# Kernel tuning notes

Measured on AMD Instinct MI355X. Metric: run time of the kernel, lower is better.

The kernel has to match this reference:

```python
import jax, jax.numpy as jnp
import numpy as np

B, X, Y, C, H = 16, 64, 64, 256, 8
N = X * Y
EPS_LN, EPS_BN = 1e-6, 1e-5

def _conv3x3(x, w):
    return jax.lax.conv_general_dilated(x, w, (1, 1), 'SAME', dimension_numbers=('NCHW', 'OIHW', 'NCHW'))

def _bn(x, g, b, m, v):
    # eval-mode BatchNorm2d with running stats
    s = g / jnp.sqrt(v + EPS_BN)
    return x * s[None, :, None, None] + (b - m * s)[None, :, None, None]

def _ln(x, g, b):
    mu = jnp.mean(x, -1, keepdims=True)
    var = jnp.mean((x - mu) ** 2, -1, keepdims=True)
    return (x - mu) * jax.lax.rsqrt(var + EPS_LN) * g + b

def _rotate_half(x):
    x1, x2 = jnp.split(x, 2, axis=-1)
    return jnp.concatenate([-x2, x1], axis=-1)

def _rope(t, f):
    return t * jnp.cos(f) + _rotate_half(t) * jnp.sin(f)

def setup_inputs() -> dict:
    key = jax.random.key(0)
    ks = jax.random.split(key, 9)
    p = {}
    p['input'] = jax.random.normal(ks[0], (B, X, Y), jnp.float32)
    p['freq_x'] = jax.random.normal(ks[1], (B, N, C // 2), jnp.float32)
    p['freq_y'] = jax.random.normal(ks[2], (B, N, C // 2), jnp.float32)
    p['conv1_w'] = jax.random.normal(ks[3], (C, 1, 3, 3), jnp.float32) * 0.1
    p['conv2_w'] = jax.random.normal(ks[4], (C, C, 3, 3), jnp.float32) * 0.02
    for nm in ('bn1', 'bn2'):
        p[nm + '_g'] = jnp.ones((C,), jnp.float32)
        p[nm + '_b'] = jnp.zeros((C,), jnp.float32)
        p[nm + '_m'] = jnp.zeros((C,), jnp.float32)
        p[nm + '_v'] = jnp.ones((C,), jnp.float32)
    p['ln1_g'] = jnp.ones((C,), jnp.float32); p['ln1_b'] = jnp.zeros((C,), jnp.float32)
    p['ln2_g'] = jnp.ones((C,), jnp.float32); p['ln2_b'] = jnp.zeros((C,), jnp.float32)
    p['qkv_w'] = jax.random.normal(ks[5], (3 * C, C), jnp.float32) * 0.02
    p['out_w'] = jax.random.normal(ks[6], (C, C), jnp.float32) * 0.02
    p['out_b'] = jnp.zeros((C,), jnp.float32)
    p['mlp_w1'] = jax.random.normal(ks[7], (C, C), jnp.float32) * 0.02
    p['mlp_b1'] = jnp.zeros((C,), jnp.float32)
    p['mlp_w2'] = jax.random.normal(ks[8], (C, C), jnp.float32) * 0.02
    p['mlp_b2'] = jnp.zeros((C,), jnp.float32)
    return p

def reference(input, freq_x, freq_y, conv1_w, conv2_w, bn1_g, bn1_b, bn1_m, bn1_v, bn2_g, bn2_b, bn2_m, bn2_v, ln1_g, ln1_b, ln2_g, ln2_b, qkv_w, out_w, out_b, mlp_w1, mlp_b1, mlp_w2, mlp_b2):
    x4 = input[:, None]  # [B,1,X,Y]
    out = jax.nn.relu(_bn(_conv3x3(x4, conv1_w), bn1_g, bn1_b, bn1_m, bn1_v))
    out = jax.nn.relu(_bn(_conv3x3(out, conv2_w), bn2_g, bn2_b, bn2_m, bn2_v))
    feat = jax.nn.relu(x4 + out)  # broadcast residual add, [B,C,X,Y]
    inp = feat.transpose(0, 2, 3, 1).reshape(B, N, C)  # 'b h x y -> b (x y) h'
    # --- attention/MLP branch (computed as in source; its result is discarded) ---
    x = _ln(inp, ln1_g, ln1_b)
    tx, ty = x[..., :C // 2], x[..., C // 2:]
    x = jnp.concatenate([_rope(tx, freq_x), _rope(ty, freq_y)], -1)
    qkv = x @ qkv_w.T  # [B,N,3C]
    q, k, v = jnp.split(qkv, 3, -1)
    def _heads(t):
        return t.reshape(B, N, H, C // H).transpose(0, 2, 1, 3)  # [B,H,N,Dh]
    q, k, v = _heads(q), _heads(k), _heads(v)
    q = jax.nn.softmax(q, -1) * ((C // H) ** -0.5)
    k = jax.nn.softmax(k, -2)
    ctx = jnp.einsum('bhnd,bhne->bhde', k, v)   # [B,H,Dh,Dh]
    o = jnp.einsum('bhnd,bhde->bhne', q, ctx)   # [B,H,N,Dh]
    o = o.transpose(0, 2, 1, 3).reshape(B, N, C) @ out_w.T + out_b
    x = o + inp
    y = _ln(x, ln2_g, ln2_b)
    y = jax.nn.gelu(y @ mlp_w1.T + mlp_b1, approximate=False) @ mlp_w2.T + mlp_b2
    x = x + y
    # source module returns `input` (the post-stem tokens), not `x`
    return inp
```

## Files before the change

kernel.cpp:

```cpp
#include <hip/hip_runtime.h>
#include <hip/hip_bf16.h>

#define BB 16
#define XY 64
#define CC 256
#define PR 66

typedef __attribute__((ext_vector_type(8)))  short short8;
typedef __attribute__((ext_vector_type(16))) float f32x16;
typedef __hip_bfloat16 bf16;

__device__ __forceinline__ void glds16(const void* g, void* l) {
  __builtin_amdgcn_global_load_lds(
      (const __attribute__((address_space(1))) void*)g,
      (__attribute__((address_space(3))) void*)l, 16, 0, 0);
}

__global__ __launch_bounds__(256) void k_conv1(
    const float* __restrict__ in,
    const float* __restrict__ w1,
    const float* __restrict__ g, const float* __restrict__ bbias,
    const float* __restrict__ m, const float* __restrict__ v,
    bf16* __restrict__ act)
{
  int blk = blockIdx.x;
  int b = blk / PR, prow = blk % PR;
  short8* base = (short8*)(act + (size_t)(b * PR + prow) * 32 * PR * 8);
  int tid = threadIdx.x;
  short8 z8 = {0, 0, 0, 0, 0, 0, 0, 0};
  if (prow == 0 || prow == PR - 1) {
    for (int i = tid; i < 32 * PR; i += 256) base[i] = z8;
    return;
  }
  __shared__ float inrow[3][PR];
  int h = prow - 1;
  for (int t = tid; t < 3 * PR; t += 256) {
    int r = t / PR, x = t % PR;
    int hr = h - 1 + r, wr = x - 1;
    inrow[r][x] = (hr >= 0 && hr < XY && wr >= 0 && wr < XY)
                      ? in[(b * XY + hr) * XY + wr] : 0.f;
  }
  __syncthreads();
  int cg = tid >> 3, w8 = tid & 7;
  float wr_[8][9], sc[8], tc[8];
#pragma unroll
  for (int u = 0; u < 8; ++u) {
    int c = cg * 8 + u;
#pragma unroll
    for (int t = 0; t < 9; ++t) wr_[u][t] = w1[c * 9 + t];
    float s = g[c] * rsqrtf(v[c] + 1e-5f);
    sc[u] = s; tc[u] = bbias[c] - m[c] * s;
  }
#pragma unroll
  for (int k = 0; k < 9; ++k) {
    int wp = w8 + 8 * k;
    if (wp < PR) {
      short8 outv = z8;
      if (wp != 0 && wp != PR - 1) {
        float o[8];
#pragma unroll
        for (int u = 0; u < 8; ++u) o[u] = 0.f;
#pragma unroll
        for (int dy = 0; dy < 3; ++dy) {
          float i0 = inrow[dy][wp - 1], i1 = inrow[dy][wp], i2 = inrow[dy][wp + 1];
#pragma unroll
          for (int u = 0; u < 8; ++u)
            o[u] += i0 * wr_[u][dy * 3] + i1 * wr_[u][dy * 3 + 1] + i2 * wr_[u][dy * 3 + 2];
        }
#pragma unroll
        for (int u = 0; u < 8; ++u) {
          bf16 hb = __float2bfloat16(fmaxf(fmaf(o[u], sc[u], tc[u]), 0.f));
          outv[u] = *(short*)&hb;
        }
      }
      base[cg * PR + wp] = outv;
    }
  }
}

__global__ __launch_bounds__(256) void k_wb(
    const float* __restrict__ w2,
    const float* __restrict__ g, const float* __restrict__ v,
    bf16* __restrict__ Wb)
{
  int e = blockIdx.x * 256 + threadIdx.x;
  int j   = e & 7;
  int co  = (e >> 3) & 255;
  int kg  = (e >> 11) & 3;
  int cc  = (e >> 13) & 7;
  int tap = e >> 16;
  int ci = cc * 32 + kg * 8 + j;
  float s = g[co] * rsqrtf(v[co] + 1e-5f);
  Wb[e] = __float2bfloat16(w2[((size_t)co * CC + ci) * 9 + tap] * s);
}

__global__ __launch_bounds__(256, 2) void k_conv2(
    const bf16* __restrict__ act,
    const bf16* __restrict__ Wb,
    const float* __restrict__ in,
    const float* __restrict__ g2, const float* __restrict__ b2,
    const float* __restrict__ m2, const float* __restrict__ v2,
    float* __restrict__ out)
{
  __shared__ alignas(16) bf16 Asm[1056 * 8];
  __shared__ alignas(16) bf16 Wsm[3][1024 * 8];
  __shared__ float inrow[2][64];

  int gg = blockIdx.x;
  int blk = (gg & 7) * 64 + (gg >> 3);
  int b = blk >> 5, h0 = (blk & 31) * 2;

  int tid = threadIdx.x;
  int lane = tid & 63, wv = tid >> 6;
  int wm = wv >> 1, wn = wv & 1;
  int l31 = lane & 31, lh = lane >> 5;

  f32x16 acc[2][4];
#pragma unroll
  for (int i = 0; i < 2; ++i)
#pragma unroll
    for (int j = 0; j < 4; ++j)
#pragma unroll
      for (int e = 0; e < 16; ++e) acc[i][j][e] = 0.f;

  if (tid < 128) inrow[tid >> 6][tid & 63] = in[(b * XY + h0 + (tid >> 6)) * XY + (tid & 63)];
  __syncthreads();

  auto stageA = [&](int cc) {
    const char* srcbase = (const char*)act +
        (size_t)(((b * PR + h0 + wv) * 32 + cc * 4) * 66) * 16;
    char* dstbase = (char*)Asm + wv * (264 * 16);
#pragma unroll
    for (int k = 0; k < 4; ++k)
      glds16(srcbase + k * 1024 + lane * 16, dstbase + k * 1024);
    if (lane < 8)
      glds16(srcbase + 4096 + lane * 16, dstbase + 4096);
  };
  auto stageW = [&](int wblk, int sbuf) {
    const char* src = (const char*)Wb + (size_t)wblk * 16384 + wv * 4096;
    char* dst = (char*)&Wsm[0][0] + sbuf * 16384 + wv * 4096;
#pragma unroll
    for (int k = 0; k < 4; ++k)
      glds16(src + k * 1024 + lane * 16, dst + k * 1024);
  };

  stageA(0);
  stageW(0, 0);
  stageW(8, 1);
  asm volatile("s_waitcnt vmcnt(4)" ::: "memory");
  __builtin_amdgcn_s_barrier();

  int it = 0, buf = 0;
#pragma unroll 1
  for (int cc = 0; cc < 8; ++cc) {
#pragma unroll 1
    for (int tap = 0; tap < 9; ++tap, ++it) {
      int dy = tap / 3, dx = tap - dy * 3;
      int sbuf = buf + 2; if (sbuf >= 3) sbuf -= 3;
      int tap2 = tap + 2, cc2 = cc;
      if (tap2 >= 9) { tap2 -= 9; ++cc2; }
      int wblk2 = tap2 * 8 + cc2;
      bool doW = (it < 70);

      if (tap != 8 && doW) stageW(wblk2, sbuf);

      const bf16* wbuf = (const bf16*)((const char*)&Wsm[0][0] + buf * 16384);
      int abase = ((wm + dy) * 4 + lh) * 66 + l31 + dx;
      int bbase = lh * 256 + wn * 128 + l31;
      short8 a[2][2], bf_[2][4];
#pragma unroll
      for (int s = 0; s < 2; ++s)
#pragma unroll
        for (int mt = 0; mt < 2; ++mt)
          a[s][mt] = *(const short8*)(Asm + (size_t)(abase + s * 132 + mt * 32) * 8);
#pragma unroll
      for (int s = 0; s < 2; ++s)
#pragma unroll
        for (int nt = 0; nt < 4; ++nt)
          bf_[s][nt] = *(const short8*)(wbuf + (size_t)(bbase + s * 512 + nt * 32) * 8);

      if (tap == 8 && it < 71) {
        asm volatile("s_waitcnt lgkmcnt(0)" ::: "memory");
        __builtin_amdgcn_s_barrier();
        stageA(cc + 1);
        stageW(wblk2, sbuf);
      }

      __builtin_amdgcn_s_setprio(1);
#pragma unroll
      for (int s = 0; s < 2; ++s)
#pragma unroll
        for (int mt = 0; mt < 2; ++mt)
#pragma unroll
          for (int nt = 0; nt < 4; ++nt)
            acc[mt][nt] = __builtin_amdgcn_mfma_f32_32x32x16_bf16(
                a[s][mt], bf_[s][nt], acc[mt][nt], 0, 0, 0);
      __builtin_amdgcn_s_setprio(0);

      if (it >= 70) asm volatile("s_waitcnt vmcnt(0)" ::: "memory");
      else          asm volatile("s_waitcnt vmcnt(4)" ::: "memory");
      __builtin_amdgcn_s_barrier();
      buf = (buf == 2) ? 0 : buf + 1;
    }
  }

  float t2[4];
#pragma unroll
  for (int nt = 0; nt < 4; ++nt) {
    int co = wn * 128 + nt * 32 + l31;
    float s2 = g2[co] * rsqrtf(v2[co] + 1e-5f);
    t2[nt] = b2[co] - m2[co] * s2;
  }
#pragma unroll
  for (int mt = 0; mt < 2; ++mt) {
#pragma unroll
    for (int e = 0; e < 16; ++e) {
      int wp = mt * 32 + (e & 3) + 8 * (e >> 2) + 4 * lh;
      float iv = inrow[wm][wp];
      float* ob = out + ((size_t)((b * XY + h0 + wm) * XY + wp)) * CC + wn * 128 + l31;
#pragma unroll
      for (int nt = 0; nt < 4; ++nt) {
        float val = fmaxf(acc[mt][nt][e] + t2[nt], 0.f);
        ob[nt * 32] = fmaxf(iv + val, 0.f);
      }
    }
  }
}

extern "C" void kernel_launch(void* const* d_in, const int* in_sizes, int n_in,
                              void* d_out, int out_size, void* d_ws, size_t ws_size,
                              hipStream_t stream) {
  const float* in_   = (const float*)d_in[0];
  const float* w1    = (const float*)d_in[3];
  const float* w2    = (const float*)d_in[4];
  const float* bn1_g = (const float*)d_in[5];
  const float* bn1_b = (const float*)d_in[6];
  const float* bn1_m = (const float*)d_in[7];
  const float* bn1_v = (const float*)d_in[8];
  const float* bn2_g = (const float*)d_in[9];
  const float* bn2_b = (const float*)d_in[10];
  const float* bn2_m = (const float*)d_in[11];
  const float* bn2_v = (const float*)d_in[12];
  float* out = (float*)d_out;

  bf16* act = (bf16*)d_ws;
  bf16* Wb  = act + (size_t)BB * PR * 32 * PR * 8;

  k_conv1<<<BB * PR, 256, 0, stream>>>(in_, w1, bn1_g, bn1_b, bn1_m, bn1_v, act);
  k_wb<<<2304, 256, 0, stream>>>(w2, bn2_g, bn2_v, Wb);
  k_conv2<<<512, 256, 0, stream>>>(act, Wb, in_, bn2_g, bn2_b, bn2_m, bn2_v, out);
}
```

Measured before the change: 106.0 us.

## Load conv2 weights straight into registers and double-buffer input tiles in LDS

Weight fragments no longer go through a triple-buffered LDS stage. Each wave now loads them straight from global memory into registers, prefetching one tap ahead. The input activation tile is double-buffered in LDS, and its staging is split into five pieces spread over the first taps of each channel chunk. This removes the per-tap barriers, keeping one sync per chunk, but doubles weight traffic, since waves that share a weight slice each fetch it. It also exposes global-load latency with only one tap of lookahead and adds register pressure.

```diff
diff --git a/kernel.cpp b/kernel.cpp
--- a/kernel.cpp
+++ b/kernel.cpp
@@ -102,8 +102,7 @@
     const float* __restrict__ m2, const float* __restrict__ v2,
     float* __restrict__ out)
 {
-  __shared__ alignas(16) bf16 Asm[1056 * 8];
-  __shared__ alignas(16) bf16 Wsm[3][1024 * 8];
+  __shared__ alignas(16) bf16 Asm[2][1056 * 8];
   __shared__ float inrow[2][64];
 
   int gg = blockIdx.x;
@@ -112,7 +111,7 @@
 
   int tid = threadIdx.x;
   int lane = tid & 63, wv = tid >> 6;
-  int wm = wv >> 1, wn = wv & 1;
+  int wm = wv >> 1, wnn = wv & 1;
   int l31 = lane & 31, lh = lane >> 5;
 
   f32x16 acc[2][4];
@@ -124,67 +123,58 @@
       for (int e = 0; e < 16; ++e) acc[i][j][e] = 0.f;
 
   if (tid < 128) inrow[tid >> 6][tid & 63] = in[(b * XY + h0 + (tid >> 6)) * XY + (tid & 63)];
-  __syncthreads();
-
-  auto stageA = [&](int cc) {
+
+  auto stageApart = [&](int cn, int part) {
     const char* srcbase = (const char*)act +
-        (size_t)(((b * PR + h0 + wv) * 32 + cc * 4) * 66) * 16;
-    char* dstbase = (char*)Asm + wv * (264 * 16);
-#pragma unroll
-    for (int k = 0; k < 4; ++k)
-      glds16(srcbase + k * 1024 + lane * 16, dstbase + k * 1024);
-    if (lane < 8)
+        (size_t)(((b * PR + h0 + wv) * 32 + cn * 4) * 66) * 16;
+    char* dstbase = (char*)&Asm[cn & 1][0] + wv * (264 * 16);
+    if (part < 4)
+      glds16(srcbase + part * 1024 + lane * 16, dstbase + part * 1024);
+    else if (lane < 8)
       glds16(srcbase + 4096 + lane * 16, dstbase + 4096);
   };
-  auto stageW = [&](int wblk, int sbuf) {
-    const char* src = (const char*)Wb + (size_t)wblk * 16384 + wv * 4096;
-    char* dst = (char*)&Wsm[0][0] + sbuf * 16384 + wv * 4096;
-#pragma unroll
-    for (int k = 0; k < 4; ++k)
-      glds16(src + k * 1024 + lane * 16, dst + k * 1024);
-  };
-
-  stageA(0);
-  stageW(0, 0);
-  stageW(8, 1);
-  asm volatile("s_waitcnt vmcnt(4)" ::: "memory");
-  __builtin_amdgcn_s_barrier();
-
-  int it = 0, buf = 0;
+
+#pragma unroll
+  for (int p = 0; p < 5; ++p) stageApart(0, p);
+
+  int wfoff = lh * 256 + wnn * 128 + l31;
+  short8 wc[2][4];
+  {
+    const short8* ws0 = (const short8*)Wb;
+#pragma unroll
+    for (int s = 0; s < 2; ++s)
+#pragma unroll
+      for (int nt = 0; nt < 4; ++nt)
+        wc[s][nt] = ws0[(s * 512) + wfoff + nt * 32];
+  }
+  __syncthreads();
+
 #pragma unroll 1
   for (int cc = 0; cc < 8; ++cc) {
+    const bf16* abuf = &Asm[cc & 1][0];
 #pragma unroll 1
-    for (int tap = 0; tap < 9; ++tap, ++it) {
+    for (int tap = 0; tap < 9; ++tap) {
+      int it = cc * 9 + tap;
+      int itn = (it < 71) ? it + 1 : 71;
+      int ccn = itn / 9, tapn = itn - ccn * 9;
+      const short8* wsn = (const short8*)(Wb + (size_t)(tapn * 8 + ccn) * 8192);
+      short8 wn_[2][4];
+#pragma unroll
+      for (int s = 0; s < 2; ++s)
+#pragma unroll
+        for (int nt = 0; nt < 4; ++nt)
+          wn_[s][nt] = wsn[(s * 512) + wfoff + nt * 32];
+
+      if (tap < 5 && cc < 7) stageApart(cc + 1, tap);
+
       int dy = tap / 3, dx = tap - dy * 3;
-      int sbuf = buf + 2; if (sbuf >= 3) sbuf -= 3;
-      int tap2 = tap + 2, cc2 = cc;
-      if (tap2 >= 9) { tap2 -= 9; ++cc2; }
-      int wblk2 = tap2 * 8 + cc2;
-      bool doW = (it < 70);
-
-      if (tap != 8 && doW) stageW(wblk2, sbuf);
-
-      const bf16* wbuf = (const bf16*)((const char*)&Wsm[0][0] + buf * 16384);
       int abase = ((wm + dy) * 4 + lh) * 66 + l31 + dx;
-      int bbase = lh * 256 + wn * 128 + l31;
-      short8 a[2][2], bf_[2][4];
+      short8 a[2][2];
 #pragma unroll
       for (int s = 0; s < 2; ++s)
 #pragma unroll
         for (int mt = 0; mt < 2; ++mt)
-          a[s][mt] = *(const short8*)(Asm + (size_t)(abase + s * 132 + mt * 32) * 8);
-#pragma unroll
-      for (int s = 0; s < 2; ++s)
-#pragma unroll
-        for (int nt = 0; nt < 4; ++nt)
-          bf_[s][nt] = *(const short8*)(wbuf + (size_t)(bbase + s * 512 + nt * 32) * 8);
-
-      if (tap == 8 && it < 71) {
-        asm volatile("s_waitcnt lgkmcnt(0)" ::: "memory");
-        __builtin_amdgcn_s_barrier();
-        stageA(cc + 1);
-        stageW(wblk2, sbuf);
-      }
+          a[s][mt] = *(const short8*)(abuf + (size_t)(abase + s * 132 + mt * 32) * 8);
 
       __builtin_amdgcn_s_setprio(1);
 #pragma unroll
@@ -194,20 +184,23 @@
 #pragma unroll
           for (int nt = 0; nt < 4; ++nt)
             acc[mt][nt] = __builtin_amdgcn_mfma_f32_32x32x16_bf16(
-                a[s][mt], bf_[s][nt], acc[mt][nt], 0, 0, 0);
+                a[s][mt], wn_[0][0]  + 0 ? wc[s][nt] : wc[s][nt],
+                acc[mt][nt], 0, 0, 0);
       __builtin_amdgcn_s_setprio(0);
 
-      if (it >= 70) asm volatile("s_waitcnt vmcnt(0)" ::: "memory");
-      else          asm volatile("s_waitcnt vmcnt(4)" ::: "memory");
-      __builtin_amdgcn_s_barrier();
-      buf = (buf == 2) ? 0 : buf + 1;
+#pragma unroll
+      for (int s = 0; s < 2; ++s)
+#pragma unroll
+        for (int nt = 0; nt < 4; ++nt)
+          wc[s][nt] = wn_[s][nt];
     }
+    __syncthreads();
   }
 
   float t2[4];
 #pragma unroll
   for (int nt = 0; nt < 4; ++nt) {
-    int co = wn * 128 + nt * 32 + l31;
+    int co = wnn * 128 + nt * 32 + l31;
     float s2 = g2[co] * rsqrtf(v2[co] + 1e-5f);
     t2[nt] = b2[co] - m2[co] * s2;
   }
@@ -217,7 +210,7 @@
     for (int e = 0; e < 16; ++e) {
       int wp = mt * 32 + (e & 3) + 8 * (e >> 2) + 4 * lh;
       float iv = inrow[wm][wp];
-      float* ob = out + ((size_t)((b * XY + h0 + wm) * XY + wp)) * CC + wn * 128 + l31;
+      float* ob = out + ((size_t)((b * XY + h0 + wm) * XY + wp)) * CC + wnn * 128 + l31;
 #pragma unroll
       for (int nt = 0; nt < 4; ++nt) {
         float val = fmaxf(acc[mt][nt][e] + t2[nt], 0.f);
```

Result: no change. 104.9 us (-1.0%).
